# Performance work log

Hardware: AMD Instinct MI355X
Metric: run time of the kernel (lower is better)

## Reference

```python
import jax, jax.numpy as jnp
import numpy as np

N, E, IN_CH, OUT_CH = 20000, 10000, 128, 64


def setup_inputs() -> dict:
    key = jax.random.key(0)
    k1, k2, k3 = jax.random.split(key, 3)
    x = jax.random.normal(k1, (N, IN_CH), dtype=jnp.float32)
    # Uniform(0,1) incidence: strictly positive degrees, same math as weighted H.
    H = jax.random.uniform(k2, (N, E), dtype=jnp.float32)
    theta = jax.random.normal(k3, (IN_CH, OUT_CH), dtype=jnp.float32) * (1.0 / np.sqrt(IN_CH))
    return {"x": x, "H": H, "theta": theta}


def reference(x, H, theta):
    # x: [N, in_ch], H: [N, E], theta: [in_ch, out_ch]
    x = x @ theta                              # [N, out_ch]
    # gen_hyedge_ft: (H @ inv(diag(colsum(H)))).T @ x == (H.T @ x) / de[:, None]
    de = jnp.sum(H, axis=0)                    # [E] hyperedge degrees
    edge_ft = (H.T @ x) / de[:, None]          # [E, out_ch]
    # gen_node_ft: inv(diag(rowsum(H))) @ H @ edge_ft == (H @ edge_ft) / dn[:, None]
    dn = jnp.sum(H, axis=1)                    # [N] node degrees
    node_ft = (H @ edge_ft) / dn[:, None]      # [N, out_ch]
    return node_ft
```

## Files before the change

### kernel.cpp

```cpp
#include <hip/hip_runtime.h>


#define N_ROWS 20000
#define E_COLS 10000
#define ETILE  128
#define E_PAD2 10112
#define OUT_CH 64

typedef __attribute__((ext_vector_type(4))) float f32x4;
typedef __attribute__((ext_vector_type(8))) short s16x8;

__device__ __forceinline__ unsigned short f2bf(float f) {
  unsigned int u = __float_as_uint(f);
  u += 0x7FFFu + ((u >> 16) & 1u);
  return (unsigned short)(u >> 16);
}

__global__ __launch_bounds__(256) void k1_xwt(const float* __restrict__ x,
                                              const float* __restrict__ theta,
                                              unsigned short* __restrict__ xwT) {
  __shared__ float xt[64][129];
  const int n0 = blockIdx.x * 64;
  const int t  = threadIdx.x;
  #pragma unroll
  for (int i = 0; i < 8; ++i) {
    int f  = t + 256 * i;
    int r  = f >> 5;
    int c4 = (f & 31) * 4;
    float4 v = make_float4(0.f, 0.f, 0.f, 0.f);
    if (n0 + r < N_ROWS) v = *(const float4*)&x[(long)(n0 + r) * 128 + c4];
    xt[r][c4] = v.x; xt[r][c4 + 1] = v.y; xt[r][c4 + 2] = v.z; xt[r][c4 + 3] = v.w;
  }
  __syncthreads();
  const int nl = t & 63;
  const int cg = t >> 6;
  const int n  = n0 + nl;
  float acc[16];
  #pragma unroll
  for (int i = 0; i < 16; ++i) acc[i] = 0.f;
  #pragma unroll 4
  for (int k = 0; k < 128; ++k) {
    float xv = xt[nl][k];
    const float* th = theta + k * 64 + cg * 16;
    #pragma unroll
    for (int i = 0; i < 16; ++i) acc[i] += xv * th[i];
  }
  if (n < N_ROWS) {
    #pragma unroll
    for (int i = 0; i < 16; ++i)
      xwT[(long)(cg * 16 + i) * N_ROWS + n] = f2bf(acc[i]);
  }
}

__global__ __launch_bounds__(256) void k2_edge(const float* __restrict__ H,
                                               const unsigned short* __restrict__ xwT,
                                               float* __restrict__ eacc,
                                               float* __restrict__ de) {
  __shared__ float tile[32][ETILE + 4];
  const int b  = blockIdx.x;
  const int et = b % 79, s = b / 79;
  const int e0 = et * ETILE;
  const int t  = threadIdx.x;
  const int w  = t >> 6;
  const int l  = t & 63;
  const int q  = l >> 4, eL = l & 15;

  const int sr = t >> 5;
  const int sc = (t & 31) * 4;
  const int eg = e0 + sc;
  const bool egv = (eg < E_COLS);
  const f32x4 z4 = {0, 0, 0, 0};

  f32x4 acc[2][4];
  #pragma unroll
  for (int sub = 0; sub < 2; ++sub)
    #pragma unroll
    for (int ct = 0; ct < 4; ++ct) acc[sub][ct] = z4;
  float deP[2] = {0.f, 0.f};

  const int c0 = 25 * s, c1 = c0 + 25;

  f32x4 pv[4];
  #pragma unroll
  for (int i = 0; i < 4; ++i)
    pv[i] = egv ? *(const f32x4*)&H[(long)(c0 * 32 + sr + 8 * i) * E_COLS + eg] : z4;

  for (int kk = c0; kk < c1; ++kk) {
    const int nb = kk * 32;
    #pragma unroll
    for (int i = 0; i < 4; ++i)
      *(f32x4*)&tile[sr + 8 * i][sc] = pv[i];
    __syncthreads();
    if (kk + 1 < c1) {
      #pragma unroll
      for (int i = 0; i < 4; ++i)
        pv[i] = egv ? *(const f32x4*)&H[(long)(nb + 32 + sr + 8 * i) * E_COLS + eg] : z4;
    }
    s16x8 af[4];
    #pragma unroll
    for (int ct = 0; ct < 4; ++ct)
      af[ct] = *(const s16x8*)&xwT[(long)(ct * 16 + eL) * N_ROWS + nb + 8 * q];
    #pragma unroll
    for (int sub = 0; sub < 2; ++sub) {
      const int ec = 32 * w + 16 * sub + eL;
      union { s16x8 v8; unsigned short u[8]; } bf;
      float ds = 0.f;
      #pragma unroll
      for (int j = 0; j < 8; ++j) {
        float v = tile[8 * q + j][ec];
        ds += v;
        bf.u[j] = f2bf(v);
      }
      deP[sub] += ds;
      #pragma unroll
      for (int ct = 0; ct < 4; ++ct)
        acc[sub][ct] = __builtin_amdgcn_mfma_f32_16x16x32_bf16(af[ct], bf.v8, acc[sub][ct], 0, 0, 0);
    }
    __syncthreads();
  }
  #pragma unroll
  for (int sub = 0; sub < 2; ++sub)
    #pragma unroll
    for (int ct = 0; ct < 4; ++ct)
      #pragma unroll
      for (int r = 0; r < 4; ++r) {
        int c = ct * 16 + q * 4 + r;
        int e = e0 + 32 * w + 16 * sub + eL;
        atomicAdd(&eacc[(long)c * E_PAD2 + e], acc[sub][ct][r]);
      }
  #pragma unroll
  for (int sub = 0; sub < 2; ++sub) {
    float d = deP[sub];
    d += __shfl_xor(d, 16, 64);
    d += __shfl_xor(d, 32, 64);
    if (l < 16) atomicAdd(&de[e0 + 32 * w + 16 * sub + l], d);
  }
}

__global__ __launch_bounds__(256) void k3_edgefin(const float* __restrict__ eacc,
                                                  const float* __restrict__ de,
                                                  unsigned short* __restrict__ eT) {
  const int e = blockIdx.x * 256 + threadIdx.x;
  const int c = blockIdx.y;
  if (e >= E_PAD2) return;
  float v = 0.f;
  if (e < E_COLS) v = eacc[(long)c * E_PAD2 + e] / de[e];
  eT[(long)c * E_PAD2 + e] = f2bf(v);
}

__global__ __launch_bounds__(64) void k4_node(const float* __restrict__ H,
                                              const unsigned short* __restrict__ eT,
                                              float* __restrict__ outacc,
                                              float* __restrict__ dn) {
  const int b  = blockIdx.x;
  const int mt = b % 1250, s = b / 1250;
  const int n0 = mt * 16;
  const int l  = threadIdx.x;
  const int q  = l >> 4, nL = l & 15;
  f32x4 acc[4] = {{0,0,0,0},{0,0,0,0},{0,0,0,0},{0,0,0,0}};
  float dnP = 0.f;
  const float* __restrict__ Hrow = H + (long)(n0 + nL) * E_COLS;
  const int k0 = s * 79, k1 = k0 + 79;
  const f32x4 z4 = {0, 0, 0, 0};
  for (int kk = k0; kk < k1; ++kk) {
    const int ec = kk * 32 + q * 8;
    f32x4 v0 = (ec     < E_COLS) ? *(const f32x4*)(Hrow + ec)     : z4;
    f32x4 v1 = (ec + 4 < E_COLS) ? *(const f32x4*)(Hrow + ec + 4) : z4;
    dnP += v0[0] + v0[1] + v0[2] + v0[3] + v1[0] + v1[1] + v1[2] + v1[3];
    union { s16x8 v8; unsigned short u[8]; } af;
    #pragma unroll
    for (int j = 0; j < 4; ++j) { af.u[j] = f2bf(v0[j]); af.u[4 + j] = f2bf(v1[j]); }
    #pragma unroll
    for (int ct = 0; ct < 4; ++ct) {
      s16x8 bf = *(const s16x8*)&eT[(long)(ct * 16 + nL) * E_PAD2 + ec];
      acc[ct] = __builtin_amdgcn_mfma_f32_16x16x32_bf16(af.v8, bf, acc[ct], 0, 0, 0);
    }
  }
  #pragma unroll
  for (int ct = 0; ct < 4; ++ct)
    #pragma unroll
    for (int r = 0; r < 4; ++r)
      atomicAdd(&outacc[(long)(n0 + q * 4 + r) * OUT_CH + ct * 16 + nL], acc[ct][r]);
  dnP += __shfl_xor(dnP, 16, 64);
  dnP += __shfl_xor(dnP, 32, 64);
  if (l < 16) atomicAdd(&dn[n0 + l], dnP);
}

__global__ __launch_bounds__(256) void k5_nodefin(float* __restrict__ out,
                                                  const float* __restrict__ dn) {
  const int idx = blockIdx.x * 256 + threadIdx.x;
  out[idx] = out[idx] / dn[idx >> 6];
}

extern "C" void kernel_launch(void* const* d_in, const int* in_sizes, int n_in,
                              void* d_out, int out_size, void* d_ws, size_t ws_size,
                              hipStream_t stream) {
  const float* x     = (const float*)d_in[0];
  const float* H     = (const float*)d_in[1];
  const float* theta = (const float*)d_in[2];
  float* out = (float*)d_out;
  char* ws = (char*)d_ws;

  const size_t OFF_XWT  = 0;
  const size_t OFF_EACC = 2560000;
  const size_t OFF_DE   = OFF_EACC + 2588672;
  const size_t OFF_DN   = OFF_DE + 40448;
  const size_t OFF_ET   = OFF_DN + 80128;

  unsigned short* xwT  = (unsigned short*)(ws + OFF_XWT);
  float*          eacc = (float*)(ws + OFF_EACC);
  float*          de   = (float*)(ws + OFF_DE);
  float*          dn   = (float*)(ws + OFF_DN);
  unsigned short* eT   = (unsigned short*)(ws + OFF_ET);

  hipMemsetAsync(eacc, 0, 2588672, stream);
  hipMemsetAsync(de,   0, 40448,   stream);
  hipMemsetAsync(dn,   0, 80000,   stream);
  hipMemsetAsync(out,  0, (size_t)out_size * sizeof(float), stream);

  k1_xwt<<<313, 256, 0, stream>>>(x, theta, xwT);
  k2_edge<<<1975, 256, 0, stream>>>(H, xwT, eacc, de);
  k3_edgefin<<<dim3(40, 64), 256, 0, stream>>>(eacc, de, eT);
  k4_node<<<5000, 64, 0, stream>>>(H, eT, out, dn);
  k5_nodefin<<<5000, 256, 0, stream>>>(out, dn);
}
```

Measured before the change: 1.408 ms.

## Deepen H prefetch pipelines in edge and node kernels, swizzle edge LDS tile

The edge-aggregation kernel now keeps two register buffers of H rows in flight, prefetching two chunks ahead, instead of one. It also replaces LDS row padding with an XOR column swizzle to avoid bank conflicts. The node-aggregation kernel now works on 128-column chunks with a double-buffered register prefetch, so global loads of the next chunk overlap the MFMA work on the current one. Both aim to hide the global-memory latency of streaming the large H matrix. The cost is higher register pressure, which may lower occupancy.

Result: faster. 1.378 ms (-2.2%).

```diff
diff --git a/kernel.cpp b/kernel.cpp
--- a/kernel.cpp
+++ b/kernel.cpp
@@ -56,7 +56,7 @@
                                                const unsigned short* __restrict__ xwT,
                                                float* __restrict__ eacc,
                                                float* __restrict__ de) {
-  __shared__ float tile[32][ETILE + 4];
+  __shared__ float tile[32][ETILE];
   const int b  = blockIdx.x;
   const int et = b % 79, s = b / 79;
   const int e0 = et * ETILE;
@@ -80,44 +80,55 @@
 
   const int c0 = 25 * s, c1 = c0 + 25;
 
-  f32x4 pv[4];
-  #pragma unroll
-  for (int i = 0; i < 4; ++i)
-    pv[i] = egv ? *(const f32x4*)&H[(long)(c0 * 32 + sr + 8 * i) * E_COLS + eg] : z4;
-
-  for (int kk = c0; kk < c1; ++kk) {
-    const int nb = kk * 32;
-    #pragma unroll
-    for (int i = 0; i < 4; ++i)
-      *(f32x4*)&tile[sr + 8 * i][sc] = pv[i];
-    __syncthreads();
-    if (kk + 1 < c1) {
-      #pragma unroll
-      for (int i = 0; i < 4; ++i)
-        pv[i] = egv ? *(const f32x4*)&H[(long)(nb + 32 + sr + 8 * i) * E_COLS + eg] : z4;
-    }
-    s16x8 af[4];
-    #pragma unroll
-    for (int ct = 0; ct < 4; ++ct)
-      af[ct] = *(const s16x8*)&xwT[(long)(ct * 16 + eL) * N_ROWS + nb + 8 * q];
-    #pragma unroll
-    for (int sub = 0; sub < 2; ++sub) {
-      const int ec = 32 * w + 16 * sub + eL;
-      union { s16x8 v8; unsigned short u[8]; } bf;
-      float ds = 0.f;
-      #pragma unroll
-      for (int j = 0; j < 8; ++j) {
-        float v = tile[8 * q + j][ec];
-        ds += v;
-        bf.u[j] = f2bf(v);
-      }
-      deP[sub] += ds;
-      #pragma unroll
-      for (int ct = 0; ct < 4; ++ct)
-        acc[sub][ct] = __builtin_amdgcn_mfma_f32_16x16x32_bf16(af[ct], bf.v8, acc[sub][ct], 0, 0, 0);
-    }
-    __syncthreads();
-  }
+  f32x4 pva[4], pvb[4];
+  #pragma unroll
+  for (int i = 0; i < 4; ++i) {
+    pva[i] = egv ? *(const f32x4*)&H[(long)(c0 * 32 + sr + 8 * i) * E_COLS + eg] : z4;
+    pvb[i] = egv ? *(const f32x4*)&H[(long)((c0 + 1) * 32 + sr + 8 * i) * E_COLS + eg] : z4;
+  }
+
+  int kk = c0;
+#define K2_STEP(PV)                                                                     \
+  {                                                                                     \
+    _Pragma("unroll")                                                                   \
+    for (int i = 0; i < 4; ++i)                                                         \
+      *(f32x4*)&tile[sr + 8 * i][(((t & 31) ^ (i << 2)) << 2)] = PV[i];                 \
+    __syncthreads();                                                                    \
+    if (kk + 2 < c1) {                                   \
+      _Pragma("unroll")                                                                 \
+      for (int i = 0; i < 4; ++i)                                                       \
+        PV[i] = egv ? *(const f32x4*)&H[(long)((kk + 2) * 32 + sr + 8 * i) * E_COLS + eg] : z4; \
+    }                                                                                   \
+    s16x8 af[4];                                                                        \
+    _Pragma("unroll")                                                                   \
+    for (int ct = 0; ct < 4; ++ct)                                                      \
+      af[ct] = *(const s16x8*)&xwT[(long)(ct * 16 + eL) * N_ROWS + kk * 32 + 8 * q];    \
+    _Pragma("unroll")                                                                   \
+    for (int sub = 0; sub < 2; ++sub) {                                                 \
+      const int ec  = 32 * w + 16 * sub + eL;                                           \
+      const int csw = (((ec >> 2) ^ (q << 2)) << 2) | (ec & 3);                         \
+      union { s16x8 v8; unsigned short u[8]; } bf;                                      \
+      float ds = 0.f;                                                                   \
+      _Pragma("unroll")                                                                 \
+      for (int j = 0; j < 8; ++j) {                                                     \
+        float v = tile[8 * q + j][csw];                                                 \
+        ds += v;                                                                        \
+        bf.u[j] = f2bf(v);                                                              \
+      }                                                                                 \
+      deP[sub] += ds;                                                                   \
+      _Pragma("unroll")                                                                 \
+      for (int ct = 0; ct < 4; ++ct)                                                    \
+        acc[sub][ct] = __builtin_amdgcn_mfma_f32_16x16x32_bf16(af[ct], bf.v8, acc[sub][ct], 0, 0, 0); \
+    }                                                                                   \
+    __syncthreads();                                                                    \
+    ++kk;                                                                               \
+  }
+
+  #pragma unroll 1
+  for (int it = 0; it < 12; ++it) { K2_STEP(pva); K2_STEP(pvb); }
+  K2_STEP(pva);
+#undef K2_STEP
+
   #pragma unroll
   for (int sub = 0; sub < 2; ++sub)
     #pragma unroll
@@ -160,22 +171,50 @@
   f32x4 acc[4] = {{0,0,0,0},{0,0,0,0},{0,0,0,0},{0,0,0,0}};
   float dnP = 0.f;
   const float* __restrict__ Hrow = H + (long)(n0 + nL) * E_COLS;
-  const int k0 = s * 79, k1 = k0 + 79;
   const f32x4 z4 = {0, 0, 0, 0};
-  for (int kk = k0; kk < k1; ++kk) {
-    const int ec = kk * 32 + q * 8;
-    f32x4 v0 = (ec     < E_COLS) ? *(const f32x4*)(Hrow + ec)     : z4;
-    f32x4 v1 = (ec + 4 < E_COLS) ? *(const f32x4*)(Hrow + ec + 4) : z4;
-    dnP += v0[0] + v0[1] + v0[2] + v0[3] + v1[0] + v1[1] + v1[2] + v1[3];
-    union { s16x8 v8; unsigned short u[8]; } af;
-    #pragma unroll
-    for (int j = 0; j < 4; ++j) { af.u[j] = f2bf(v0[j]); af.u[4 + j] = f2bf(v1[j]); }
-    #pragma unroll
-    for (int ct = 0; ct < 4; ++ct) {
-      s16x8 bf = *(const s16x8*)&eT[(long)(ct * 16 + nL) * E_PAD2 + ec];
-      acc[ct] = __builtin_amdgcn_mfma_f32_16x16x32_bf16(af.v8, bf, acc[ct], 0, 0, 0);
-    }
-  }
+  const int cb0 = s * 20;
+  const int cb1 = (cb0 + 20 < 79) ? (cb0 + 20) : 79;
+
+#define K4_LOAD(V, CB)                                                   \
+  { _Pragma("unroll")                                                    \
+    for (int u = 0; u < 8; ++u) {                                        \
+      const int col = (CB) * 128 + (u >> 1) * 32 + q * 8 + (u & 1) * 4;  \
+      V[u] = (col < E_COLS) ? *(const f32x4*)(Hrow + col) : z4;          \
+    } }
+
+#define K4_CONSUME(V, CB)                                                \
+  { _Pragma("unroll")                                                    \
+    for (int kc = 0; kc < 4; ++kc) {                                     \
+      const int ec = (CB) * 128 + kc * 32 + q * 8;                       \
+      union { s16x8 v8; unsigned short u[8]; } af;                       \
+      _Pragma("unroll")                                                  \
+      for (int j = 0; j < 4; ++j) {                                      \
+        float av = V[2 * kc][j], cv = V[2 * kc + 1][j];                  \
+        dnP += av + cv;                                                  \
+        af.u[j] = f2bf(av); af.u[4 + j] = f2bf(cv);                      \
+      }                                                                  \
+      _Pragma("unroll")                                                  \
+      for (int ct = 0; ct < 4; ++ct) {                                   \
+        s16x8 bf = *(const s16x8*)&eT[(long)(ct * 16 + nL) * E_PAD2 + ec]; \
+        acc[ct] = __builtin_amdgcn_mfma_f32_16x16x32_bf16(af.v8, bf, acc[ct], 0, 0, 0); \
+      }                                                                  \
+    } }
+
+  f32x4 va[8], vb[8];
+  K4_LOAD(va, cb0);
+  int cb = cb0, rem = cb1 - cb0;
+  while (rem >= 2) {
+    K4_LOAD(vb, cb + 1);
+    K4_CONSUME(va, cb);
+    ++cb; --rem;
+    if (rem >= 2) { K4_LOAD(va, cb + 1); }
+    K4_CONSUME(vb, cb);
+    ++cb; --rem;
+  }
+  if (rem) { K4_CONSUME(va, cb); }
+#undef K4_LOAD
+#undef K4_CONSUME
+
   #pragma unroll
   for (int ct = 0; ct < 4; ++ct)
     #pragma unroll
```
